# Optimization experiments

Hardware: AMD Instinct MI355X
Metric: run time of the kernel (lower is better)

## Reference

```python
import jax, jax.numpy as jnp
import numpy as np
from jax import lax


def loo_max(x):
    """Leave-one-out max over axis 1. x: (N, L, D) -> (N, L, D).
    Equivalent to torch's repeat + strip_main_diagonal + max(dim=2) without the
    (N, L, L, D) intermediate: for position i the LOO max is top1 unless i is
    the (unique chosen) argmax, in which case it is top2. With duplicates the
    second top-k value equals top1, so the result is still exact.
    """
    xt = jnp.swapaxes(x, 1, 2)                 # (N, D, L)
    top2, _ = lax.top_k(xt, 2)                 # (N, D, 2)
    amax = jnp.argmax(xt, axis=-1)             # (N, D)
    idx = jnp.arange(x.shape[1])[None, :, None]  # (1, L, 1)
    top1 = top2[..., 0][:, None, :]            # (N, 1, D)
    second = top2[..., 1][:, None, :]          # (N, 1, D)
    return jnp.where(idx == amax[:, None, :], second, top1)


def cross_max(y, from_length):
    """Plain max-pool over axis 1 of y, broadcast to (N, from_length, D)."""
    m = jnp.max(y, axis=1)                     # (N, D)
    return jnp.broadcast_to(m[:, None, :], (y.shape[0], from_length, y.shape[2]))


def setup_inputs() -> dict:
    key = jax.random.key(0)
    ks = jax.random.split(key, 6)
    N, L0, L1, D = 16, 2048, 1024, 128
    H = D + 2 * D  # in_dim + sum(in_dims) = 384
    scale = 1.0 / np.sqrt(H)
    return {
        "x0": jax.random.normal(ks[0], (N, L0, D), jnp.float32),
        "x1": jax.random.normal(ks[1], (N, L1, D), jnp.float32),
        "W0": jax.random.normal(ks[2], (D, H), jnp.float32) * scale,
        "b0": jax.random.normal(ks[3], (D,), jnp.float32) * scale,
        "W1": jax.random.normal(ks[4], (D, H), jnp.float32) * scale,
        "b1": jax.random.normal(ks[5], (D,), jnp.float32) * scale,
    }


def reference(x0, x1, W0, b0, W1, b1):
    L0, L1 = x0.shape[1], x1.shape[1]
    # group 0: [x0 | LOO-max(x0) | max(x1) broadcast] -> linear
    c0 = jnp.concatenate([x0, loo_max(x0), cross_max(x1, L0)], axis=-1)  # (N, L0, 384)
    y0 = jnp.einsum('nlh,oh->nlo', c0, W0) + b0                           # (N, L0, 128)
    # group 1: [x1 | max(x0) broadcast | LOO-max(x1)] -> linear
    c1 = jnp.concatenate([x1, cross_max(x0, L1), loo_max(x1)], axis=-1)  # (N, L1, 384)
    y1 = jnp.einsum('nlh,oh->nlo', c1, W1) + b1                           # (N, L1, 128)
    return (y0, y1)
```

## Files before the change

kernel.cpp:

```cpp
#include <hip/hip_runtime.h>
#include <hip/hip_bf16.h>

#define N_  16
#define L0_ 2048
#define L1_ 1024
#define D_  128
#define H_  384

#define PM1_0 0
#define PM2_0 65536
#define PAM_0 131072
#define PM1_1 196608
#define PM2_1 229376
#define PAM_1 262144
#define BASE_ 294912
#define WBF_  299008
#define HCNT_ 315392
#define HLIST_ 316160

typedef float  floatx4  __attribute__((ext_vector_type(4)));
typedef __bf16 bf16x8   __attribute__((ext_vector_type(8)));
typedef unsigned short ushortx8 __attribute__((ext_vector_type(8)));

__device__ __forceinline__ unsigned short f2bf(float f) {
  union { float f; unsigned int u; } v; v.f = f;
  unsigned int u = v.u;
  return (unsigned short)((u + 0x7fffu + ((u >> 16) & 1u)) >> 16);
}

__global__ __launch_bounds__(256) void stats_kernel(
    const float* __restrict__ x0, const float* __restrict__ x1,
    float* __restrict__ ws) {
  __shared__ float sm1[8][128], sm2[8][128];
  __shared__ int   sam[8][128];
  int bid = blockIdx.x, tid = threadIdx.x;
  const float* x; int n, chunk, L; float *pm1, *pm2; int* pam;
  if (bid < 512) {
    x = x0; n = bid >> 5; chunk = bid & 31; L = L0_;
    pm1 = ws + PM1_0; pm2 = ws + PM2_0; pam = (int*)ws + PAM_0;
  } else {
    int b = bid - 512;
    x = x1; n = b >> 4; chunk = b & 15; L = L1_;
    pm1 = ws + PM1_1; pm2 = ws + PM2_1; pam = (int*)ws + PAM_1;
  }
  int q = tid & 31, sub = tid >> 5;
  int lbase = chunk * 64 + sub * 8;
  const float* xp = x + (size_t)(n * L + lbase) * D_ + q * 4;

  float m1[4], m2[4]; int am[4];
#pragma unroll
  for (int j = 0; j < 4; j++) { m1[j] = -3.4e38f; m2[j] = -3.4e38f; am[j] = 0; }
#pragma unroll
  for (int r = 0; r < 8; r++) {
    float4 v = *(const float4*)(xp + (size_t)r * D_);
    float vv[4] = { v.x, v.y, v.z, v.w };
    int l = lbase + r;
#pragma unroll
    for (int j = 0; j < 4; j++) {
      if (vv[j] > m1[j]) { m2[j] = m1[j]; m1[j] = vv[j]; am[j] = l; }
      else if (vv[j] > m2[j]) m2[j] = vv[j];
    }
  }
#pragma unroll
  for (int j = 0; j < 4; j++) {
    int d = q * 4 + j;
    sm1[sub][d] = m1[j]; sm2[sub][d] = m2[j]; sam[sub][d] = am[j];
  }
  __syncthreads();
  if (tid < 128) {
    int d = tid;
    float M1 = sm1[0][d], M2 = sm2[0][d]; int AM = sam[0][d];
#pragma unroll
    for (int s = 1; s < 8; s++) {
      float c1 = sm1[s][d];
      if (c1 > M1) { M2 = fmaxf(M1, sm2[s][d]); M1 = c1; AM = sam[s][d]; }
      else M2 = fmaxf(M2, c1);
    }
    int idx = (chunk * N_ + n) * D_ + d;
    pm1[idx] = M1; pm2[idx] = M2; pam[idx] = AM;
  }
}

__global__ __launch_bounds__(256) void prep_kernel(
    const float* __restrict__ W0, const float* __restrict__ b0,
    const float* __restrict__ W1, const float* __restrict__ b1,
    float* __restrict__ ws) {
  __shared__ float t1a[128], t1b[128], sdl[128], bpart[128];
  __shared__ int   sam2[128], scnt[32];
  int bid = blockIdx.x, tid = threadIdx.x;
  int g = bid >> 4, n = bid & 15;
  const float* W = g ? W1 : W0;
  const float* bias = g ? b1 : b0;

  if (tid < 32) scnt[tid] = 0;

  if (tid < 128) {
    int d = tid;
    const float* pm1 = ws + PM1_0; const float* pm2 = ws + PM2_0;
    const int* pam = (int*)ws + PAM_0;
    float M1 = pm1[n * D_ + d], M2 = pm2[n * D_ + d]; int AM = pam[n * D_ + d];
    for (int c = 1; c < 32; c++) {
      int id2 = (c * N_ + n) * D_ + d;
      float c1 = pm1[id2];
      if (c1 > M1) { M2 = fmaxf(M1, pm2[id2]); M1 = c1; AM = pam[id2]; }
      else M2 = fmaxf(M2, c1);
    }
    t1a[d] = M1;
    if (g == 0) { sdl[d] = M2 - M1; sam2[d] = AM; }
  } else {
    int d = tid - 128;
    const float* pm1 = ws + PM1_1; const float* pm2 = ws + PM2_1;
    const int* pam = (int*)ws + PAM_1;
    float M1 = pm1[n * D_ + d], M2 = pm2[n * D_ + d]; int AM = pam[n * D_ + d];
    for (int c = 1; c < 16; c++) {
      int id2 = (c * N_ + n) * D_ + d;
      float c1 = pm1[id2];
      if (c1 > M1) { M2 = fmaxf(M1, pm2[id2]); M1 = c1; AM = pam[id2]; }
      else M2 = fmaxf(M2, c1);
    }
    t1b[d] = M1;
    if (g == 1) { sdl[d] = M2 - M1; sam2[d] = AM; }
  }
  __syncthreads();

  int o = tid & 127, half = tid >> 7;
  {
    const float* wr = W + (size_t)o * H_ + 128 + half * 128;
    const float* tv = half ? t1b : t1a;
    float bsum = 0.f;
#pragma unroll 4
    for (int d = 0; d < 128; d += 4) {
      float4 wv = *(const float4*)(wr + d);
      bsum += tv[d] * wv.x + tv[d + 1] * wv.y + tv[d + 2] * wv.z + tv[d + 3] * wv.w;
    }
    if (half) { bpart[o] = bsum; }
    __syncthreads();
    if (!half) ws[BASE_ + (g * N_ + n) * D_ + o] = bias[o] + bsum + bpart[o];
  }

  if (tid < 128) {
    int d = tid; int am = sam2[d]; float dl = sdl[d];
    int t = am >> 6;
    int slot = atomicAdd(&scnt[t], 1);
    int tile = (g == 0) ? (n * 32 + t) : (512 + n * 16 + t);
    int* hl = (int*)ws + HLIST_ + tile * 256;
    hl[slot * 2]     = (am & 63) | (d << 8);
    hl[slot * 2 + 1] = __float_as_int(dl);
  }
  __syncthreads();
  int tcount = g ? 16 : 32;
  if (tid < tcount) {
    int tile = (g == 0) ? (n * 32 + tid) : (512 + n * 16 + tid);
    ((int*)ws)[HCNT_ + tile] = scnt[tid];
  }

  if (n == 0) {
    unsigned short* wbf = (unsigned short*)(ws + WBF_) + g * 16384;
#pragma unroll
    for (int it = 0; it < 64; it++) {
      int f = tid + 256 * it;
      int oo = f >> 7, k = f & 127;
      wbf[f] = f2bf(W[(size_t)oo * H_ + k]);
    }
  }
}

__global__ __launch_bounds__(256) void gemm_kernel(
    const float* __restrict__ x0, const float* __restrict__ x1,
    const float* __restrict__ W0, const float* __restrict__ W1,
    float* __restrict__ out, const float* __restrict__ ws) {
  int bid = blockIdx.x, tid = threadIdx.x;
  int g, n, r0, L; const float *x, *W; float* y;
  if (bid < 512) { g = 0; n = bid >> 5; r0 = (bid & 31) << 6; L = L0_; x = x0; W = W0; y = out; }
  else { int b = bid - 512; g = 1; n = b >> 4; r0 = (b & 15) << 6; L = L1_; x = x1; W = W1;
         y = out + (size_t)N_ * L0_ * D_; }

  int w = tid >> 6, lane = tid & 63, lm = lane & 15, lq = lane >> 4;
  int rsub = (w & 1) << 5, cw = (w >> 1) << 6;

  int hc = ((const int*)ws)[HCNT_ + bid];
  const int* hl = (const int*)ws + HLIST_ + bid * 256;
  const float* bp = ws + BASE_ + (g * N_ + n) * D_;
  float bb[4];
#pragma unroll
  for (int j = 0; j < 4; j++) bb[j] = bp[cw + j * 16 + lm];

  const unsigned short* wbf = (const unsigned short*)(ws + WBF_) + g * 16384;
  const float* xb = x + (size_t)(n * L + r0 + rsub) * D_;

  floatx4 acc[2][4];
#pragma unroll
  for (int i = 0; i < 2; i++)
#pragma unroll
    for (int j = 0; j < 4; j++) acc[i][j] = (floatx4){0.f, 0.f, 0.f, 0.f};

#pragma unroll 1
  for (int kk = 0; kk < 4; kk++) {
    int ko = kk * 32 + lq * 8;
    bf16x8 af[2];
#pragma unroll
    for (int i = 0; i < 2; i++) {
      const float* p = xb + (size_t)(i * 16 + lm) * D_ + ko;
      float4 u = *(const float4*)p;
      float4 v = *(const float4*)(p + 4);
      ushortx8 t = { f2bf(u.x), f2bf(u.y), f2bf(u.z), f2bf(u.w),
                     f2bf(v.x), f2bf(v.y), f2bf(v.z), f2bf(v.w) };
      af[i] = __builtin_bit_cast(bf16x8, t);
    }
    bf16x8 bfr[4];
#pragma unroll
    for (int j = 0; j < 4; j++)
      bfr[j] = __builtin_bit_cast(bf16x8,
          *(const ushortx8*)&wbf[(cw + j * 16 + lm) * 128 + ko]);
#pragma unroll
    for (int i = 0; i < 2; i++)
#pragma unroll
      for (int j = 0; j < 4; j++)
        acc[i][j] = __builtin_amdgcn_mfma_f32_16x16x32_bf16(af[i], bfr[j], acc[i][j], 0, 0, 0);
  }

  int off = 128 + (g << 7);
  for (int k = 0; k < hc; k++) {
    int e = hl[2 * k]; float dl = __int_as_float(hl[2 * k + 1]);
    int row = e & 63, d = e >> 8;
    int rl = row - rsub;
    if (rl >= 0 && rl < 32 && ((rl >> 2) & 3) == lq) {
      int i = rl >> 4, rr = rl & 3;
#pragma unroll
      for (int j = 0; j < 4; j++)
        acc[i][j][rr] += dl * W[(size_t)(cw + j * 16 + lm) * H_ + off + d];
    }
  }

  float* yb = y + (size_t)(n * L + r0 + rsub) * D_;
#pragma unroll
  for (int i = 0; i < 2; i++)
#pragma unroll
    for (int j = 0; j < 4; j++)
#pragma unroll
      for (int r = 0; r < 4; r++)
        yb[(size_t)(i * 16 + lq * 4 + r) * D_ + cw + j * 16 + lm] = acc[i][j][r] + bb[j];
}

extern "C" void kernel_launch(void* const* d_in, const int* in_sizes, int n_in,
                              void* d_out, int out_size, void* d_ws, size_t ws_size,
                              hipStream_t stream) {
  const float* x0 = (const float*)d_in[0];
  const float* x1 = (const float*)d_in[1];
  const float* W0 = (const float*)d_in[2];
  const float* b0 = (const float*)d_in[3];
  const float* W1 = (const float*)d_in[4];
  const float* b1 = (const float*)d_in[5];
  float* out = (float*)d_out;
  float* ws  = (float*)d_ws;

  hipLaunchKernelGGL(stats_kernel, dim3(768), dim3(256), 0, stream, x0, x1, ws);
  hipLaunchKernelGGL(prep_kernel,  dim3(32),  dim3(256), 0, stream, W0, b0, W1, b1, ws);
  hipLaunchKernelGGL(gemm_kernel,  dim3(768), dim3(256), 0, stream,
                     x0, x1, W0, W1, out, ws);
}
```

Measured before the change: 137.0 us.

## Transpose GEMM tiling so each wave owns 16 rows and writes float4 outputs

Each wave now handles 16 full rows across all 128 output columns. The x fragments are loaded and converted once up front as the MFMA B operand, and the bf16 weights become the A operand, so the accumulator layout gives each lane four contiguous output columns. Outputs and bias are then stored and loaded as float4, replacing strided scalar stores, and x is no longer read redundantly by two waves. The cost is more weight-fragment loads per wave and a heavier LOO correction loop per matching lane.

```diff
diff --git a/kernel.cpp b/kernel.cpp
--- a/kernel.cpp
+++ b/kernel.cpp
@@ -176,70 +176,61 @@
          y = out + (size_t)N_ * L0_ * D_; }
 
   int w = tid >> 6, lane = tid & 63, lm = lane & 15, lq = lane >> 4;
-  int rsub = (w & 1) << 5, cw = (w >> 1) << 6;
-
-  int hc = ((const int*)ws)[HCNT_ + bid];
-  const int* hl = (const int*)ws + HLIST_ + bid * 256;
-  const float* bp = ws + BASE_ + (g * N_ + n) * D_;
-  float bb[4];
-#pragma unroll
-  for (int j = 0; j < 4; j++) bb[j] = bp[cw + j * 16 + lm];
-
+  int lbase = r0 + w * 16;
+  const float* xb = x + (size_t)(n * L + lbase) * D_;
   const unsigned short* wbf = (const unsigned short*)(ws + WBF_) + g * 16384;
-  const float* xb = x + (size_t)(n * L + r0 + rsub) * D_;
-
-  floatx4 acc[2][4];
-#pragma unroll
-  for (int i = 0; i < 2; i++)
-#pragma unroll
-    for (int j = 0; j < 4; j++) acc[i][j] = (floatx4){0.f, 0.f, 0.f, 0.f};
+
+  bf16x8 bfr[4];
+#pragma unroll
+  for (int kk = 0; kk < 4; kk++) {
+    const float* p = xb + (size_t)lm * D_ + kk * 32 + lq * 8;
+    float4 u = *(const float4*)p;
+    float4 v = *(const float4*)(p + 4);
+    ushortx8 t = { f2bf(u.x), f2bf(u.y), f2bf(u.z), f2bf(u.w),
+                   f2bf(v.x), f2bf(v.y), f2bf(v.z), f2bf(v.w) };
+    bfr[kk] = __builtin_bit_cast(bf16x8, t);
+  }
+
+  floatx4 acc[8];
+#pragma unroll
+  for (int j = 0; j < 8; j++) acc[j] = (floatx4){0.f, 0.f, 0.f, 0.f};
 
 #pragma unroll 1
   for (int kk = 0; kk < 4; kk++) {
     int ko = kk * 32 + lq * 8;
-    bf16x8 af[2];
-#pragma unroll
-    for (int i = 0; i < 2; i++) {
-      const float* p = xb + (size_t)(i * 16 + lm) * D_ + ko;
-      float4 u = *(const float4*)p;
-      float4 v = *(const float4*)(p + 4);
-      ushortx8 t = { f2bf(u.x), f2bf(u.y), f2bf(u.z), f2bf(u.w),
-                     f2bf(v.x), f2bf(v.y), f2bf(v.z), f2bf(v.w) };
-      af[i] = __builtin_bit_cast(bf16x8, t);
-    }
-    bf16x8 bfr[4];
-#pragma unroll
-    for (int j = 0; j < 4; j++)
-      bfr[j] = __builtin_bit_cast(bf16x8,
-          *(const ushortx8*)&wbf[(cw + j * 16 + lm) * 128 + ko]);
-#pragma unroll
-    for (int i = 0; i < 2; i++)
-#pragma unroll
-      for (int j = 0; j < 4; j++)
-        acc[i][j] = __builtin_amdgcn_mfma_f32_16x16x32_bf16(af[i], bfr[j], acc[i][j], 0, 0, 0);
-  }
-
+#pragma unroll
+    for (int j = 0; j < 8; j++) {
+      bf16x8 a = __builtin_bit_cast(bf16x8,
+          *(const ushortx8*)&wbf[(j * 16 + lm) * 128 + ko]);
+      acc[j] = __builtin_amdgcn_mfma_f32_16x16x32_bf16(a, bfr[kk], acc[j], 0, 0, 0);
+    }
+  }
+
+  int hc = ((const int*)ws)[HCNT_ + bid];
+  const int* hl = (const int*)ws + HLIST_ + bid * 256;
   int off = 128 + (g << 7);
   for (int k = 0; k < hc; k++) {
     int e = hl[2 * k]; float dl = __int_as_float(hl[2 * k + 1]);
     int row = e & 63, d = e >> 8;
-    int rl = row - rsub;
-    if (rl >= 0 && rl < 32 && ((rl >> 2) & 3) == lq) {
-      int i = rl >> 4, rr = rl & 3;
-#pragma unroll
-      for (int j = 0; j < 4; j++)
-        acc[i][j][rr] += dl * W[(size_t)(cw + j * 16 + lm) * H_ + off + d];
-    }
-  }
-
-  float* yb = y + (size_t)(n * L + r0 + rsub) * D_;
-#pragma unroll
-  for (int i = 0; i < 2; i++)
-#pragma unroll
-    for (int j = 0; j < 4; j++)
-#pragma unroll
-      for (int r = 0; r < 4; r++)
-        yb[(size_t)(i * 16 + lq * 4 + r) * D_ + cw + j * 16 + lm] = acc[i][j][r] + bb[j];
+    if ((row >> 4) == w && (row & 15) == lm) {
+#pragma unroll
+      for (int j = 0; j < 8; j++)
+#pragma unroll
+        for (int r = 0; r < 4; r++)
+          acc[j][r] += dl * W[(size_t)(j * 16 + lq * 4 + r) * H_ + off + d];
+    }
+  }
+
+  const float* bp = ws + BASE_ + (g * N_ + n) * D_;
+  float* yb = y + (size_t)(n * L + lbase + lm) * D_;
+#pragma unroll
+  for (int j = 0; j < 8; j++) {
+    float4 bb = *(const float4*)&bp[j * 16 + lq * 4];
+    float4 o4;
+    o4.x = acc[j][0] + bb.x; o4.y = acc[j][1] + bb.y;
+    o4.z = acc[j][2] + bb.z; o4.w = acc[j][3] + bb.w;
+    *(float4*)&yb[j * 16 + lq * 4] = o4;
+  }
 }
 
 extern "C" void kernel_launch(void* const* d_in, const int* in_sizes, int n_in,
```

Measured after the change: 137.9 us. No clear change (+0.7%).
